# Kernel tuning notes

Hardware: AMD Instinct MI355X
Metric: run time of the kernel (lower is better)

The kernel has to match this reference:

```python
import jax, jax.numpy as jnp
import numpy as np

N = 25000          # nodes
E = 400000         # edges (avg degree 16)
H = 64             # hidden_nf
TYPE_DIM = 1
NL = 5             # 4 gcl layers + dgcl_0 (identical shapes, stacked)
GROUP = jnp.array([[[1., 0.], [0., 1.]], [[-1., 0.], [0., -1.]]], dtype=jnp.float32)  # [G,2,2]


def setup_inputs() -> dict:
    key = jax.random.key(0)
    ks = iter(jax.random.split(key, 40))
    def nrm(shape, scale=0.05):
        return jax.random.normal(next(ks), shape, dtype=jnp.float32) * scale
    inp = {}
    inp["nodes"] = nrm((N, 4 + TYPE_DIM), 1.0)
    inp["edges"] = jax.random.randint(next(ks), (2, E), 0, N)
    inp["edge_attr"] = nrm((E, 1), 1.0)
    # embedding: Linear(input_dim, H)
    inp["W_emb"] = nrm((4 + TYPE_DIM, H)); inp["b_emb"] = jnp.zeros((H,), jnp.float32)
    # group_mlp: Linear(G*H, H) -> SiLU -> Linear(H, H)
    G = GROUP.shape[0]
    inp["Wg1"] = nrm((G * H, H)); inp["bg1"] = jnp.zeros((H,), jnp.float32)
    inp["Wg2"] = nrm((H, H));     inp["bg2"] = jnp.zeros((H,), jnp.float32)
    # stacked GCL params for gcl_0..3 + dgcl_0 (all H->H, edges_in_nf=1)
    inp["eW1"] = nrm((NL, 2 * H + 1, H)); inp["eb1"] = jnp.zeros((NL, H), jnp.float32)
    inp["eW2"] = nrm((NL, H, H));         inp["eb2"] = jnp.zeros((NL, H), jnp.float32)
    inp["nW1"] = nrm((NL, 2 * H, H));     inp["nb1"] = jnp.zeros((NL, H), jnp.float32)
    inp["nW2"] = nrm((NL, H, H));         inp["nb2"] = jnp.zeros((NL, H), jnp.float32)
    # dgcl_1: GCL(H, 2*len(group)=4, H)
    inp["deW1"] = nrm((2 * H + 1, H)); inp["deb1"] = jnp.zeros((H,), jnp.float32)
    inp["deW2"] = nrm((H, H));         inp["deb2"] = jnp.zeros((H,), jnp.float32)
    inp["dnW1"] = nrm((2 * H, H));     inp["dnb1"] = jnp.zeros((H,), jnp.float32)
    inp["dnW2"] = nrm((H, 2 * G));     inp["dnb2"] = jnp.zeros((2 * G,), jnp.float32)
    return inp


def _gcl(h, row, col, edge_attr, eW1, eb1, eW2, eb2, nW1, nb1, nW2, nb2):
    # edge model: gather -> MLP (Linear,SiLU,Linear,SiLU)
    e_in = jnp.concatenate([h[row], h[col], edge_attr], axis=1)  # [E, 2H+1]
    e = jax.nn.silu(e_in @ eW1 + eb1)
    e = jax.nn.silu(e @ eW2 + eb2)                               # [E, H]
    # node model: scatter-sum by source index, then MLP (Linear,SiLU,Linear)
    agg = jax.ops.segment_sum(e, row, num_segments=h.shape[0])   # [N, H]
    out = jnp.concatenate([h, agg], axis=1)                      # [N, 2H]
    out = jax.nn.silu(out @ nW1 + nb1) @ nW2 + nb2
    return out  # recurrent=False: no residual


def reference(nodes, edges, edge_attr, W_emb, b_emb, Wg1, bg1, Wg2, bg2,
              eW1, eb1, eW2, eb2, nW1, nb1, nW2, nb2,
              deW1, deb1, deW2, deb2, dnW1, dnb1, dnW2, dnb2):
    loc, vel, ntype = nodes[:, :2], nodes[:, 2:4], nodes[:, 4:]
    # group-equivariant embedding: transform loc/vel by each group element
    loc_g = jnp.einsum('nd,gde->gne', loc, GROUP)   # [G, N, 2]
    vel_g = jnp.einsum('nd,gde->gne', vel, GROUP)   # [G, N, 2]
    ntype_g = jnp.broadcast_to(ntype, (GROUP.shape[0],) + ntype.shape)
    feats = jnp.concatenate([loc_g, vel_g, ntype_g], axis=2)   # [G, N, 5]
    h_g = feats @ W_emb + b_emb                                 # [G, N, H]
    h = jnp.transpose(h_g, (1, 0, 2)).reshape(nodes.shape[0], -1)  # [N, G*H]
    h = jax.nn.silu(h @ Wg1 + bg1) @ Wg2 + bg2
    row, col = edges[0], edges[1]
    for i in range(eW1.shape[0]):  # gcl_0..3 then dgcl_0
        h = _gcl(h, row, col, edge_attr, eW1[i], eb1[i], eW2[i], eb2[i],
                 nW1[i], nb1[i], nW2[i], nb2[i])
    # dgcl_1: node output dim = 2*len(group)
    x = _gcl(h, row, col, edge_attr, deW1, deb1, deW2, deb2,
             dnW1, dnb1, dnW2, dnb2)
    return x
```

## Files before the change

### kernel.cpp

```cpp
#include <hip/hip_runtime.h>
#include <hip/hip_bf16.h>

#define N_NODES 25000
#define N_EDGES 400000
#define NB_SCAN ((N_NODES + 255) / 256)
#define EDGE_TILES (N_EDGES / 16)
#define TPW 2
#define EDGE_WAVES (EDGE_TILES / TPW)
#define EDGE_BLOCKS (EDGE_WAVES / 4)
#define NODE_TILES ((N_NODES + 15) / 16)
#define NODE_BLOCKS2 ((NODE_TILES + 1) / 2)

typedef __attribute__((ext_vector_type(8))) short short8;
typedef __attribute__((ext_vector_type(4))) float f32x4;

__device__ __forceinline__ float silu_f(float x) {
  return x * __builtin_amdgcn_rcpf(1.0f + __expf(-x));
}

__device__ __forceinline__ short f2bf_s(float x) {
  __hip_bfloat16 h = __float2bfloat16(x);
  return *reinterpret_cast<short*>(&h);
}
__device__ __forceinline__ float bf_s2f(short s) {
  __hip_bfloat16 h = *reinterpret_cast<__hip_bfloat16*>(&s);
  return __bfloat162float(h);
}

__device__ __forceinline__ void load_afrag(const float* T, int s, int quad, int n16,
                                           short8& ahi, short8& alo) {
#pragma unroll
  for (int j = 0; j < 8; ++j) {
    float tv = T[(s * 32 + quad * 8 + j) * 17 + n16];
    short hi = f2bf_s(tv);
    ahi[j] = hi;
    alo[j] = f2bf_s(tv - bf_s2f(hi));
  }
}
__device__ __forceinline__ void load_bfrag(const float* __restrict__ W, int k0, int col,
                                           short8& bhi, short8& blo) {
#pragma unroll
  for (int j = 0; j < 8; ++j) {
    float w = W[(k0 + j) * 64 + col];
    short hi = f2bf_s(w);
    bhi[j] = hi;
    blo[j] = f2bf_s(w - bf_s2f(hi));
  }
}
__device__ __forceinline__ f32x4 mfma3(short8 ahi, short8 alo, short8 bhi, short8 blo,
                                       f32x4 acc) {
  acc = __builtin_amdgcn_mfma_f32_16x16x32_bf16(ahi, bhi, acc, 0, 0, 0);
  acc = __builtin_amdgcn_mfma_f32_16x16x32_bf16(ahi, blo, acc, 0, 0, 0);
  acc = __builtin_amdgcn_mfma_f32_16x16x32_bf16(alo, bhi, acc, 0, 0, 0);
  return acc;
}

__global__ __launch_bounds__(256) void k_hist(const int* __restrict__ rows,
                                              int* __restrict__ counts)
{
  int stride = gridDim.x * blockDim.x;
  for (int e = blockIdx.x * blockDim.x + threadIdx.x; e < N_EDGES; e += stride)
    atomicAdd(&counts[rows[e]], 1);
}

__global__ __launch_bounds__(256) void k_scanA(const int* __restrict__ counts,
                                               int* __restrict__ bsum)
{
  __shared__ int sd[256];
  int t = threadIdx.x;
  int i = blockIdx.x * 256 + t;
  int x = (i < N_NODES) ? counts[i] : 0;
  sd[t] = x; __syncthreads();
  for (int d = 128; d > 0; d >>= 1) { if (t < d) sd[t] += sd[t + d]; __syncthreads(); }
  if (t == 0) bsum[blockIdx.x] = sd[0];
}

__global__ __launch_bounds__(128) void k_scanB(const int* __restrict__ bsum,
                                               int* __restrict__ boffs)
{
  __shared__ int buf[128];
  int t = threadIdx.x;
  int x = (t < NB_SCAN) ? bsum[t] : 0;
  buf[t] = x; __syncthreads();
  for (int d = 1; d < 128; d <<= 1) {
    int y = (t >= d) ? buf[t - d] : 0;
    __syncthreads();
    buf[t] += y;
    __syncthreads();
  }
  if (t < NB_SCAN) boffs[t] = buf[t] - x;
}

__global__ __launch_bounds__(256) void k_scanC(const int* __restrict__ counts,
                                               const int* __restrict__ boffs,
                                               int* __restrict__ cursor)
{
  __shared__ int buf[256];
  int t = threadIdx.x;
  int i = blockIdx.x * 256 + t;
  int x = (i < N_NODES) ? counts[i] : 0;
  buf[t] = x; __syncthreads();
  for (int d = 1; d < 256; d <<= 1) {
    int y = (t >= d) ? buf[t - d] : 0;
    __syncthreads();
    buf[t] += y;
    __syncthreads();
  }
  if (i < N_NODES) cursor[i] = boffs[blockIdx.x] + buf[t] - x;
}

__global__ __launch_bounds__(256) void k_scatter(
    const int* __restrict__ rows, const int* __restrict__ cols,
    const float* __restrict__ eatt, int* __restrict__ cursor,
    int* __restrict__ srow, int* __restrict__ scol, float* __restrict__ sea)
{
  int stride = gridDim.x * blockDim.x;
  for (int e = blockIdx.x * blockDim.x + threadIdx.x; e < N_EDGES; e += stride) {
    int r = rows[e];
    int pos = atomicAdd(&cursor[r], 1);
    srow[pos] = r;
    scol[pos] = cols[e];
    sea[pos] = eatt[e];
  }
}

__global__ __launch_bounds__(256) void k_w2prep(const float* __restrict__ eW2,
                                                const float* __restrict__ deW2,
                                                short* __restrict__ w2p)
{
  int layer = blockIdx.x;
  const float* src = (layer < 5) ? (eW2 + layer * 64 * 64) : deW2;
  short* dst = w2p + layer * 8192;
  for (int t = threadIdx.x; t < 4096; t += 256) {
    int j = t & 7, n16 = (t >> 3) & 15, quad = (t >> 7) & 3, nt = (t >> 9) & 3,
        s = (t >> 11) & 1;
    float val = src[(s * 32 + quad * 8 + j) * 64 + nt * 16 + n16];
    short hi = f2bf_s(val);
    short lo = f2bf_s(val - bf_s2f(hi));
    int base = ((s * 4 + nt) * 4 + quad) * 128 + n16 * 8 + j;
    dst[base] = hi;
    dst[base + 4096] = lo;
  }
}

__global__ __launch_bounds__(256, 2) void k_embed_fused(
    const float* __restrict__ nodes,
    const float* __restrict__ W_emb, const float* __restrict__ b_emb,
    const float* __restrict__ Wg1, const float* __restrict__ bg1,
    const float* __restrict__ Wg2, const float* __restrict__ bg2,
    const float* __restrict__ eW1_0, const float* __restrict__ eb1_0,
    float* __restrict__ h, float* __restrict__ u, float* __restrict__ v,
    float* __restrict__ agg)
{
  const int lane = threadIdx.x & 63;
  const int wv = threadIdx.x >> 6;
  const int n16 = lane & 15;
  const int quad = lane >> 4;
  const int col = wv * 16 + n16;

  short8 W1hi[4], W1lo[4], W2hi[2], W2lo[2], Uhi[2], Ulo[2], Vhi[2], Vlo[2];
#pragma unroll
  for (int s = 0; s < 4; ++s)
    load_bfrag(Wg1, s * 32 + quad * 8, col, W1hi[s], W1lo[s]);
#pragma unroll
  for (int s = 0; s < 2; ++s) {
    load_bfrag(Wg2, s * 32 + quad * 8, col, W2hi[s], W2lo[s]);
    load_bfrag(eW1_0, s * 32 + quad * 8, col, Uhi[s], Ulo[s]);
    load_bfrag(eW1_0 + 64 * 64, s * 32 + quad * 8, col, Vhi[s], Vlo[s]);
  }
  float bg1v = bg1[col], bg2v = bg2[col], ebv = eb1_0[col];
  float w0 = W_emb[0 * 64 + lane], w1 = W_emb[1 * 64 + lane],
        w2 = W_emb[2 * 64 + lane], w3 = W_emb[3 * 64 + lane],
        w4 = W_emb[4 * 64 + lane];
  float bev = b_emb[lane];

  __shared__ float Ta[128 * 17];
  __shared__ float Tt[64 * 17];
  __shared__ float Th[64 * 17];
  __shared__ float Tu[64 * 17];
  __shared__ float Tv[64 * 17];

  int n0 = blockIdx.x * 16;
#pragma unroll
  for (int e4 = 0; e4 < 4; ++e4) {
    int e = wv * 4 + e4;
    int n = min(n0 + e, N_NODES - 1);
    float x0 = nodes[n * 5 + 0], x1 = nodes[n * 5 + 1],
          x2 = nodes[n * 5 + 2], x3 = nodes[n * 5 + 3],
          x4 = nodes[n * 5 + 4];
    float base = bev + x4 * w4;
    float sv = x0 * w0 + x1 * w1 + x2 * w2 + x3 * w3;
    Ta[lane * 17 + e] = base + sv;
    Ta[(64 + lane) * 17 + e] = base - sv;
  }
  __syncthreads();

  f32x4 a1 = {};
#pragma unroll
  for (int s = 0; s < 4; ++s) {
    short8 ahi, alo;
    load_afrag(Ta, s, quad, n16, ahi, alo);
    a1 = mfma3(ahi, alo, W1hi[s], W1lo[s], a1);
  }
#pragma unroll
  for (int r = 0; r < 4; ++r)
    Tt[col * 17 + quad * 4 + r] = silu_f(a1[r] + bg1v);
  __syncthreads();

  f32x4 a2 = {};
#pragma unroll
  for (int s = 0; s < 2; ++s) {
    short8 ahi, alo;
    load_afrag(Tt, s, quad, n16, ahi, alo);
    a2 = mfma3(ahi, alo, W2hi[s], W2lo[s], a2);
  }
#pragma unroll
  for (int r = 0; r < 4; ++r)
    Th[col * 17 + quad * 4 + r] = a2[r] + bg2v;
  __syncthreads();

  f32x4 aU = {}, aV = {};
#pragma unroll
  for (int s = 0; s < 2; ++s) {
    short8 ahi, alo;
    load_afrag(Th, s, quad, n16, ahi, alo);
    aU = mfma3(ahi, alo, Uhi[s], Ulo[s], aU);
    aV = mfma3(ahi, alo, Vhi[s], Vlo[s], aV);
  }
#pragma unroll
  for (int r = 0; r < 4; ++r) {
    Tu[col * 17 + quad * 4 + r] = aU[r] + ebv;
    Tv[col * 17 + quad * 4 + r] = aV[r];
  }
  __syncthreads();

#pragma unroll
  for (int e4 = 0; e4 < 4; ++e4) {
    int e = wv * 4 + e4;
    int n = n0 + e;
    if (n < N_NODES) {
      h[n * 64 + lane] = Th[lane * 17 + e];
      u[n * 64 + lane] = Tu[lane * 17 + e];
      v[n * 64 + lane] = Tv[lane * 17 + e];
      agg[n * 64 + lane] = 0.f;
    }
  }
}

__global__ __launch_bounds__(256, 2) void k_postfused(
    float* __restrict__ h, float* __restrict__ agg,
    const float* __restrict__ nW1, const float* __restrict__ nb1,
    const float* __restrict__ nW2, const float* __restrict__ nb2,
    const float* __restrict__ eW1n, const float* __restrict__ eb1n,
    float* __restrict__ u, float* __restrict__ v)
{
  const int lane = threadIdx.x & 63;
  const int wv = threadIdx.x >> 6;
  const int n16 = lane & 15;
  const int quad = lane >> 4;
  const int col = wv * 16 + n16;

  short8 W1hi[4], W1lo[4], W2hi[2], W2lo[2], Uhi[2], Ulo[2], Vhi[2], Vlo[2];
#pragma unroll
  for (int s = 0; s < 4; ++s)
    load_bfrag(nW1, s * 32 + quad * 8, col, W1hi[s], W1lo[s]);
#pragma unroll
  for (int s = 0; s < 2; ++s) {
    load_bfrag(nW2, s * 32 + quad * 8, col, W2hi[s], W2lo[s]);
    load_bfrag(eW1n, s * 32 + quad * 8, col, Uhi[s], Ulo[s]);
    load_bfrag(eW1n + 64 * 64, s * 32 + quad * 8, col, Vhi[s], Vlo[s]);
  }
  float b1 = nb1[col], b2 = nb2[col], ebv = eb1n[col];

  __shared__ float LA[2][128 * 17];
  __shared__ float LB[2][64 * 17];

  int t0 = blockIdx.x * 2;
#pragma unroll
  for (int q = 0; q < 2; ++q) {
    int n0 = (t0 + q) * 16;
#pragma unroll
    for (int e4 = 0; e4 < 4; ++e4) {
      int e = wv * 4 + e4;
      int n = min(n0 + e, N_NODES - 1);
      LA[q][lane * 17 + e] = h[n * 64 + lane];
      LA[q][(64 + lane) * 17 + e] = agg[n * 64 + lane];
    }
  }
  __syncthreads();

  f32x4 a1[2] = {};
#pragma unroll
  for (int q = 0; q < 2; ++q)
#pragma unroll
    for (int s = 0; s < 4; ++s) {
      short8 ahi, alo;
      load_afrag(LA[q], s, quad, n16, ahi, alo);
      a1[q] = mfma3(ahi, alo, W1hi[s], W1lo[s], a1[q]);
    }
#pragma unroll
  for (int q = 0; q < 2; ++q)
#pragma unroll
    for (int r = 0; r < 4; ++r)
      LB[q][col * 17 + quad * 4 + r] = silu_f(a1[q][r] + b1);
  __syncthreads();

  f32x4 a2[2] = {};
#pragma unroll
  for (int q = 0; q < 2; ++q)
#pragma unroll
    for (int s = 0; s < 2; ++s) {
      short8 ahi, alo;
      load_afrag(LB[q], s, quad, n16, ahi, alo);
      a2[q] = mfma3(ahi, alo, W2hi[s], W2lo[s], a2[q]);
    }
#pragma unroll
  for (int q = 0; q < 2; ++q)
#pragma unroll
    for (int r = 0; r < 4; ++r)
      LA[q][col * 17 + quad * 4 + r] = a2[q][r] + b2;
  __syncthreads();

  f32x4 aU[2] = {}, aV[2] = {};
#pragma unroll
  for (int q = 0; q < 2; ++q)
#pragma unroll
    for (int s = 0; s < 2; ++s) {
      short8 ahi, alo;
      load_afrag(LA[q], s, quad, n16, ahi, alo);
      aU[q] = mfma3(ahi, alo, Uhi[s], Ulo[s], aU[q]);
      aV[q] = mfma3(ahi, alo, Vhi[s], Vlo[s], aV[q]);
    }
#pragma unroll
  for (int q = 0; q < 2; ++q)
#pragma unroll
    for (int r = 0; r < 4; ++r) {
      LA[q][1088 + col * 17 + quad * 4 + r] = aU[q][r] + ebv;
      LB[q][col * 17 + quad * 4 + r] = aV[q][r];
    }
  __syncthreads();

#pragma unroll
  for (int q = 0; q < 2; ++q) {
    int n0 = (t0 + q) * 16;
#pragma unroll
    for (int e4 = 0; e4 < 4; ++e4) {
      int e = wv * 4 + e4;
      int n = n0 + e;
      if (n < N_NODES) {
        h[n * 64 + lane] = LA[q][lane * 17 + e];
        u[n * 64 + lane] = LA[q][1088 + lane * 17 + e];
        v[n * 64 + lane] = LB[q][lane * 17 + e];
        agg[n * 64 + lane] = 0.f;
      }
    }
  }
}

__global__ __launch_bounds__(256) void k_edge(
    const float* __restrict__ u, const float* __restrict__ v,
    const int* __restrict__ srow, const int* __restrict__ scol,
    const float* __restrict__ sea,
    const float* __restrict__ wea,
    const short* __restrict__ w2p, const float* __restrict__ eb2,
    float* __restrict__ agg)
{
  const int lane = threadIdx.x & 63;
  const int wv = threadIdx.x >> 6;
  const int n16 = lane & 15;
  const int quad = lane >> 4;

  const short8* Wp8 = reinterpret_cast<const short8*>(w2p);
  short8 Whi[2][4], Wlo[2][4];
#pragma unroll
  for (int s = 0; s < 2; ++s)
#pragma unroll
    for (int nt = 0; nt < 4; ++nt) {
      Whi[s][nt] = Wp8[((s * 4 + nt) * 4 + quad) * 16 + n16];
      Wlo[s][nt] = Wp8[((s * 4 + nt) * 4 + quad) * 16 + n16 + 512];
    }
  float we = wea[lane];
  float b2v[4];
#pragma unroll
  for (int nt = 0; nt < 4; ++nt) b2v[nt] = eb2[nt * 16 + n16];

  __shared__ float Tl[4][64 * 17];
  float* T = Tl[wv];

  const int wid = blockIdx.x * 4 + wv;
  const int tile0 = wid * TPW;

  int cur_row = -1;
  bool first_atomic = true;
  float asum[4] = {0.f, 0.f, 0.f, 0.f};

  auto reduce_pick = [&](float a0, float a1, float a2, float a3) -> float {
    a0 += __shfl_xor(a0, 16); a0 += __shfl_xor(a0, 32);
    a1 += __shfl_xor(a1, 16); a1 += __shfl_xor(a1, 32);
    a2 += __shfl_xor(a2, 16); a2 += __shfl_xor(a2, 32);
    a3 += __shfl_xor(a3, 16); a3 += __shfl_xor(a3, 32);
    float o = a0;
    o = (quad == 1) ? a1 : o;
    o = (quad == 2) ? a2 : o;
    o = (quad == 3) ? a3 : o;
    return o;
  };

  auto gather = [&](int r16a, int c16a, float (&uuT)[16], float (&vvT)[16]) {
#pragma unroll
    for (int e = 0; e < 16; ++e) {
      int r = __builtin_amdgcn_readlane(r16a, e);
      int c = __builtin_amdgcn_readlane(c16a, e);
      uuT[e] = u[r * 64 + lane];
      vvT[e] = v[c * 64 + lane];
    }
  };

  auto phase1_mfma = [&](float ea16v, const float (&uuT)[16], const float (&vvT)[16],
                         f32x4 (&acc)[4]) {
#pragma unroll
    for (int e = 0; e < 16; ++e) {
      float ea = __int_as_float(__builtin_amdgcn_readlane(__float_as_int(ea16v), e));
      T[lane * 17 + e] = silu_f(uuT[e] + vvT[e] + ea * we);
    }
    __builtin_amdgcn_wave_barrier();
#pragma unroll
    for (int s = 0; s < 2; ++s) {
      short8 ahi, alo;
#pragma unroll
      for (int j = 0; j < 8; ++j) {
        float tv = T[(s * 32 + quad * 8 + j) * 17 + n16];
        short hi = f2bf_s(tv);
        ahi[j] = hi;
        alo[j] = f2bf_s(tv - bf_s2f(hi));
      }
#pragma unroll
      for (int nt = 0; nt < 4; ++nt) {
        acc[nt] = __builtin_amdgcn_mfma_f32_16x16x32_bf16(ahi, Whi[s][nt], acc[nt], 0, 0, 0);
        acc[nt] = __builtin_amdgcn_mfma_f32_16x16x32_bf16(ahi, Wlo[s][nt], acc[nt], 0, 0, 0);
        acc[nt] = __builtin_amdgcn_mfma_f32_16x16x32_bf16(alo, Whi[s][nt], acc[nt], 0, 0, 0);
      }
    }
    __builtin_amdgcn_wave_barrier();
  };

  auto epilogue = [&](int r16a, f32x4 (&acc)[4]) {
    float ev[4][4];
#pragma unroll
    for (int reg = 0; reg < 4; ++reg)
#pragma unroll
      for (int nt = 0; nt < 4; ++nt)
        ev[reg][nt] = silu_f(acc[nt][reg] + b2v[nt]);

    int rup = __shfl_up(r16a, 1);
    bool nf = (lane < 16) && ((lane == 0) ? (r16a != cur_row) : (r16a != rup));
    unsigned mask = (unsigned)(__ballot(nf) & 0xFFFFull);

    int s = 0;
    while (s < 16) {
      if ((mask >> s) & 1u) {
        if (cur_row >= 0) {
          float o = reduce_pick(asum[0], asum[1], asum[2], asum[3]);
          if (first_atomic) { unsafeAtomicAdd(&agg[cur_row * 64 + lane], o); first_atomic = false; }
          else agg[cur_row * 64 + lane] = o;
        }
        asum[0] = asum[1] = asum[2] = asum[3] = 0.f;
        cur_row = __shfl(r16a, s);
      }
      unsigned rem = mask & ~((2u << s) - 1u);
      int e = rem ? (__ffs(rem) - 1) : 16;
#pragma unroll
      for (int reg = 0; reg < 4; ++reg) {
        int m = quad * 4 + reg;
        bool in = (m >= s) && (m < e);
        asum[0] += in ? ev[reg][0] : 0.f;
        asum[1] += in ? ev[reg][1] : 0.f;
        asum[2] += in ? ev[reg][2] : 0.f;
        asum[3] += in ? ev[reg][3] : 0.f;
      }
      s = e;
    }
    __builtin_amdgcn_wave_barrier();
  };

  int e0 = tile0 * 16;
  int rA = srow[e0 + n16], cA = scol[e0 + n16];
  float eA = sea[e0 + n16];
  float uuA[16], vvA[16];
  gather(rA, cA, uuA, vvA);

  int e1 = e0 + 16;
  int rB = srow[e1 + n16], cB = scol[e1 + n16];
  float eB = sea[e1 + n16];

  f32x4 accA[4] = {};
  phase1_mfma(eA, uuA, vvA, accA);

  float uuB[16], vvB[16];
  gather(rB, cB, uuB, vvB);

  epilogue(rA, accA);

  f32x4 accB[4] = {};
  phase1_mfma(eB, uuB, vvB, accB);
  epilogue(rB, accB);

  if (cur_row >= 0) {
    float o = reduce_pick(asum[0], asum[1], asum[2], asum[3]);
    unsafeAtomicAdd(&agg[cur_row * 64 + lane], o);
  }
}

__global__ __launch_bounds__(256, 2) void k_final_mfma(
    const float* __restrict__ h, const float* __restrict__ agg,
    const float* __restrict__ dnW1, const float* __restrict__ dnb1,
    const float* __restrict__ dnW2, const float* __restrict__ dnb2,
    float* __restrict__ out)
{
  const int lane = threadIdx.x & 63;
  const int wv = threadIdx.x >> 6;
  const int n16 = lane & 15;
  const int quad = lane >> 4;
  const int col = wv * 16 + n16;

  short8 W1hi[4], W1lo[4];
#pragma unroll
  for (int s = 0; s < 4; ++s)
    load_bfrag(dnW1, s * 32 + quad * 8, col, W1hi[s], W1lo[s]);
  float b1 = dnb1[col];

  __shared__ float Ta[128 * 17];
  __shared__ float Tt[64 * 17];
  __shared__ float W2s[256];
  __shared__ float Tp[4][64];

  W2s[threadIdx.x] = dnW2[threadIdx.x];

  int n0 = blockIdx.x * 16;
#pragma unroll
  for (int e4 = 0; e4 < 4; ++e4) {
    int e = wv * 4 + e4;
    int n = min(n0 + e, N_NODES - 1);
    Ta[lane * 17 + e] = h[n * 64 + lane];
    Ta[(64 + lane) * 17 + e] = agg[n * 64 + lane];
  }
  __syncthreads();

  f32x4 a1 = {};
#pragma unroll
  for (int s = 0; s < 4; ++s) {
    short8 ahi, alo;
    load_afrag(Ta, s, quad, n16, ahi, alo);
    a1 = mfma3(ahi, alo, W1hi[s], W1lo[s], a1);
  }
#pragma unroll
  for (int r = 0; r < 4; ++r)
    Tt[col * 17 + quad * 4 + r] = silu_f(a1[r] + b1);
  __syncthreads();

  int m = lane >> 2, c = lane & 3;
  float p = 0.f;
#pragma unroll
  for (int kk = 0; kk < 16; ++kk) {
    int k = wv * 16 + kk;
    p += Tt[k * 17 + m] * W2s[k * 4 + c];
  }
  Tp[wv][lane] = p;
  __syncthreads();

  if (threadIdx.x < 64) {
    int n = n0 + (threadIdx.x >> 2);
    if (n < N_NODES) {
      float o = Tp[0][threadIdx.x] + Tp[1][threadIdx.x] +
                Tp[2][threadIdx.x] + Tp[3][threadIdx.x] + dnb2[threadIdx.x & 3];
      out[n * 4 + (threadIdx.x & 3)] = o;
    }
  }
}

extern "C" void kernel_launch(void* const* d_in, const int* in_sizes, int n_in,
                              void* d_out, int out_size, void* d_ws, size_t ws_size,
                              hipStream_t stream)
{
  const float* nodes = (const float*)d_in[0];
  const int*   edges = (const int*)d_in[1];
  const float* eatt  = (const float*)d_in[2];
  const float* W_emb = (const float*)d_in[3];
  const float* b_emb = (const float*)d_in[4];
  const float* Wg1   = (const float*)d_in[5];
  const float* bg1   = (const float*)d_in[6];
  const float* Wg2   = (const float*)d_in[7];
  const float* bg2   = (const float*)d_in[8];
  const float* eW1   = (const float*)d_in[9];
  const float* eb1   = (const float*)d_in[10];
  const float* eW2   = (const float*)d_in[11];
  const float* eb2   = (const float*)d_in[12];
  const float* nW1   = (const float*)d_in[13];
  const float* nb1   = (const float*)d_in[14];
  const float* nW2   = (const float*)d_in[15];
  const float* nb2   = (const float*)d_in[16];
  const float* deW1  = (const float*)d_in[17];
  const float* deb1  = (const float*)d_in[18];
  const float* deW2  = (const float*)d_in[19];
  const float* deb2  = (const float*)d_in[20];
  const float* dnW1  = (const float*)d_in[21];
  const float* dnb1  = (const float*)d_in[22];
  const float* dnW2  = (const float*)d_in[23];
  const float* dnb2  = (const float*)d_in[24];
  float* out = (float*)d_out;

  float* h   = (float*)d_ws;
  float* u   = h + N_NODES * 64;
  float* v   = u + N_NODES * 64;
  float* agg = v + N_NODES * 64;
  int* counts = (int*)(agg + N_NODES * 64);
  int* cursor = counts + N_NODES;
  int* bsum   = cursor + N_NODES;
  int* boffs  = bsum + 128;
  int* srow   = boffs + 128;
  int* scol   = srow + N_EDGES;
  float* sea  = (float*)(scol + N_EDGES);
  short* w2p  = (short*)(sea + N_EDGES);

  const int* rows = edges;
  const int* cols = edges + N_EDGES;

  hipMemsetAsync(counts, 0, N_NODES * sizeof(int), stream);
  k_w2prep<<<6, 256, 0, stream>>>(eW2, deW2, w2p);
  k_hist<<<400, 256, 0, stream>>>(rows, counts);
  k_scanA<<<NB_SCAN, 256, 0, stream>>>(counts, bsum);
  k_scanB<<<1, 128, 0, stream>>>(bsum, boffs);
  k_scanC<<<NB_SCAN, 256, 0, stream>>>(counts, boffs, cursor);
  k_scatter<<<400, 256, 0, stream>>>(rows, cols, eatt, cursor, srow, scol, sea);

  k_embed_fused<<<NODE_TILES, 256, 0, stream>>>(nodes, W_emb, b_emb, Wg1, bg1,
                                                Wg2, bg2, eW1, eb1, h, u, v, agg);

  for (int i = 0; i < 5; ++i) {
    k_edge<<<EDGE_BLOCKS, 256, 0, stream>>>(u, v, srow, scol, sea,
                                            eW1 + i * 129 * 64 + 128 * 64,
                                            w2p + i * 8192, eb2 + i * 64, agg);
    const float* eW1next = (i < 4) ? (eW1 + (i + 1) * 129 * 64) : deW1;
    const float* eb1next = (i < 4) ? (eb1 + (i + 1) * 64) : deb1;
    k_postfused<<<NODE_BLOCKS2, 256, 0, stream>>>(h, agg,
                                                  nW1 + i * 128 * 64, nb1 + i * 64,
                                                  nW2 + i * 64 * 64, nb2 + i * 64,
                                                  eW1next, eb1next, u, v);
  }
  k_edge<<<EDGE_BLOCKS, 256, 0, stream>>>(u, v, srow, scol, sea, deW1 + 128 * 64,
                                          w2p + 5 * 8192, deb2, agg);
  k_final_mfma<<<NODE_TILES, 256, 0, stream>>>(h, agg, dnW1, dnb1, dnW2, dnb2, out);
}
```

Baseline: 479.1 us.

## Gather edge operands directly in MFMA fragment layout, drop LDS transpose

The edge kernel now loads each lane's u/v row segments as float4 vectors already arranged in the MFMA A-fragment layout (row = edge n16, k = quad*8 + j). This replaces the per-element readlane gather followed by a transpose through shared memory. It removes the LDS staging buffer, its wave barriers and the scalar readlane loop, and turns 32 scalar loads into 8 vector loads per lane. The trade is that each lane now reads a different row, so a wave's accesses are less contiguous.

```diff
diff --git a/kernel.cpp b/kernel.cpp
--- a/kernel.cpp
+++ b/kernel.cpp
@@ -379,13 +379,16 @@
       Whi[s][nt] = Wp8[((s * 4 + nt) * 4 + quad) * 16 + n16];
       Wlo[s][nt] = Wp8[((s * 4 + nt) * 4 + quad) * 16 + n16 + 512];
     }
-  float we = wea[lane];
+
+  float4 weq[4];
+  weq[0] = *reinterpret_cast<const float4*>(&wea[quad * 8]);
+  weq[1] = *reinterpret_cast<const float4*>(&wea[quad * 8 + 4]);
+  weq[2] = *reinterpret_cast<const float4*>(&wea[32 + quad * 8]);
+  weq[3] = *reinterpret_cast<const float4*>(&wea[32 + quad * 8 + 4]);
+
   float b2v[4];
 #pragma unroll
   for (int nt = 0; nt < 4; ++nt) b2v[nt] = eb2[nt * 16 + n16];
-
-  __shared__ float Tl[4][64 * 17];
-  float* T = Tl[wv];
 
   const int wid = blockIdx.x * 4 + wv;
   const int tile0 = wid * TPW;
@@ -406,42 +409,42 @@
     return o;
   };
 
-  auto gather = [&](int r16a, int c16a, float (&uuT)[16], float (&vvT)[16]) {
-#pragma unroll
-    for (int e = 0; e < 16; ++e) {
-      int r = __builtin_amdgcn_readlane(r16a, e);
-      int c = __builtin_amdgcn_readlane(c16a, e);
-      uuT[e] = u[r * 64 + lane];
-      vvT[e] = v[c * 64 + lane];
-    }
+  auto gather_frag = [&](int r, int c, float4 (&uu)[4], float4 (&vv)[4]) {
+    const float* ub = u + r * 64 + quad * 8;
+    const float* vb = v + c * 64 + quad * 8;
+    uu[0] = *reinterpret_cast<const float4*>(ub);
+    uu[1] = *reinterpret_cast<const float4*>(ub + 4);
+    uu[2] = *reinterpret_cast<const float4*>(ub + 32);
+    uu[3] = *reinterpret_cast<const float4*>(ub + 36);
+    vv[0] = *reinterpret_cast<const float4*>(vb);
+    vv[1] = *reinterpret_cast<const float4*>(vb + 4);
+    vv[2] = *reinterpret_cast<const float4*>(vb + 32);
+    vv[3] = *reinterpret_cast<const float4*>(vb + 36);
   };
 
-  auto phase1_mfma = [&](float ea16v, const float (&uuT)[16], const float (&vvT)[16],
-                         f32x4 (&acc)[4]) {
-#pragma unroll
-    for (int e = 0; e < 16; ++e) {
-      float ea = __int_as_float(__builtin_amdgcn_readlane(__float_as_int(ea16v), e));
-      T[lane * 17 + e] = silu_f(uuT[e] + vvT[e] + ea * we);
-    }
-    __builtin_amdgcn_wave_barrier();
-#pragma unroll
-    for (int s = 0; s < 2; ++s) {
-      short8 ahi, alo;
-#pragma unroll
-      for (int j = 0; j < 8; ++j) {
-        float tv = T[(s * 32 + quad * 8 + j) * 17 + n16];
-        short hi = f2bf_s(tv);
-        ahi[j] = hi;
-        alo[j] = f2bf_s(tv - bf_s2f(hi));
+  auto make_frags = [&](const float4 (&uu)[4], const float4 (&vv)[4], float ea,
+                        short8 (&ahi)[2], short8 (&alo)[2]) {
+    const float* uf = reinterpret_cast<const float*>(uu);
+    const float* vf = reinterpret_cast<const float*>(vv);
+    const float* wf = reinterpret_cast<const float*>(weq);
+#pragma unroll
+    for (int k = 0; k < 16; ++k) {
+      float t = silu_f(uf[k] + vf[k] + ea * wf[k]);
+      short hi = f2bf_s(t);
+      ahi[k >> 3][k & 7] = hi;
+      alo[k >> 3][k & 7] = f2bf_s(t - bf_s2f(hi));
+    }
+  };
+
+  auto do_mfma = [&](const short8 (&ahi)[2], const short8 (&alo)[2], f32x4 (&acc)[4]) {
+#pragma unroll
+    for (int s = 0; s < 2; ++s)
+#pragma unroll
+      for (int nt = 0; nt < 4; ++nt) {
+        acc[nt] = __builtin_amdgcn_mfma_f32_16x16x32_bf16(ahi[s], Whi[s][nt], acc[nt], 0, 0, 0);
+        acc[nt] = __builtin_amdgcn_mfma_f32_16x16x32_bf16(ahi[s], Wlo[s][nt], acc[nt], 0, 0, 0);
+        acc[nt] = __builtin_amdgcn_mfma_f32_16x16x32_bf16(alo[s], Whi[s][nt], acc[nt], 0, 0, 0);
       }
-#pragma unroll
-      for (int nt = 0; nt < 4; ++nt) {
-        acc[nt] = __builtin_amdgcn_mfma_f32_16x16x32_bf16(ahi, Whi[s][nt], acc[nt], 0, 0, 0);
-        acc[nt] = __builtin_amdgcn_mfma_f32_16x16x32_bf16(ahi, Wlo[s][nt], acc[nt], 0, 0, 0);
-        acc[nt] = __builtin_amdgcn_mfma_f32_16x16x32_bf16(alo, Whi[s][nt], acc[nt], 0, 0, 0);
-      }
-    }
-    __builtin_amdgcn_wave_barrier();
   };
 
   auto epilogue = [&](int r16a, f32x4 (&acc)[4]) {
@@ -480,29 +483,32 @@
       }
       s = e;
     }
-    __builtin_amdgcn_wave_barrier();
   };
 
   int e0 = tile0 * 16;
   int rA = srow[e0 + n16], cA = scol[e0 + n16];
-  float eA = sea[e0 + n16];
-  float uuA[16], vvA[16];
-  gather(rA, cA, uuA, vvA);
+  float eaA = sea[e0 + n16];
+  float4 uuA[4], vvA[4];
+  gather_frag(rA, cA, uuA, vvA);
 
   int e1 = e0 + 16;
   int rB = srow[e1 + n16], cB = scol[e1 + n16];
-  float eB = sea[e1 + n16];
-
+  float eaB = sea[e1 + n16];
+
+  short8 ahiA[2], aloA[2];
+  make_frags(uuA, vvA, eaA, ahiA, aloA);
   f32x4 accA[4] = {};
-  phase1_mfma(eA, uuA, vvA, accA);
-
-  float uuB[16], vvB[16];
-  gather(rB, cB, uuB, vvB);
+  do_mfma(ahiA, aloA, accA);
+
+  float4 uuB[4], vvB[4];
+  gather_frag(rB, cB, uuB, vvB);
 
   epilogue(rA, accA);
 
+  short8 ahiB[2], aloB[2];
+  make_frags(uuB, vvB, eaB, ahiB, aloB);
   f32x4 accB[4] = {};
-  phase1_mfma(eB, uuB, vvB, accB);
+  do_mfma(ahiB, aloB, accB);
   epilogue(rB, accB);
 
   if (cur_row >= 0) {
```

Result: slower. 497.1 us (+3.8%).
